# Performance work log

Hardware: AMD Instinct MI355X
Metric: run time of the kernel (lower is better)

The kernel has to match this reference:

```python
import jax, jax.numpy as jnp
import numpy as np

EPS_PROX = 5.0   # proximal epsilon from __init__
BN_EPS = 1e-5    # torch BatchNorm1d default eps
STRIDE = 3


def setup_inputs() -> dict:
    key = jax.random.key(0)
    ks = jax.random.split(key, 9)
    B, T, D = 64, 768, 128     # batch, timesteps, input_size
    E, H, O, K = 64, 128, 10, 3  # embedding_dim, hidden, output, kernel
    Tc = (T - K) // STRIDE + 1   # 256 conv output steps
    s_ih = 1.0 / np.sqrt(H)
    return {
        "inputs": jax.random.normal(ks[0], (B, T, D), jnp.float32),
        "r": jax.random.normal(ks[1], (B, E, Tc), jnp.float32),
        "conv_w": jax.random.normal(ks[2], (E, D, K), jnp.float32) * (1.0 / np.sqrt(D * K)),
        "conv_b": jnp.zeros((E,), jnp.float32),
        "bn_gamma": jnp.ones((E,), jnp.float32),
        "bn_beta": jnp.zeros((E,), jnp.float32),
        "w_ih": jax.random.normal(ks[3], (4 * H, E), jnp.float32) * s_ih,
        "w_hh": jax.random.normal(ks[4], (4 * H, H), jnp.float32) * s_ih,
        "b_ih": jax.random.normal(ks[5], (4 * H,), jnp.float32) * s_ih,
        "b_hh": jax.random.normal(ks[6], (4 * H,), jnp.float32) * s_ih,
        "lin_w": jax.random.normal(ks[7], (O, H), jnp.float32) * s_ih,
        "lin_b": jnp.zeros((O,), jnp.float32),
        "batch_size": B,
    }


def _forward(inputs, conv_w, conv_b, bn_gamma, bn_beta,
             w_ih, w_hh, b_ih, b_hh, lin_w, lin_b):
    # F.normalize(inputs, dim=2): L2 normalize feature dim
    nrm = jnp.sqrt(jnp.sum(inputs * inputs, axis=2, keepdims=True))
    x = inputs / jnp.maximum(nrm, 1e-12)
    x = jnp.transpose(x, (0, 2, 1))  # [B, D, T]
    # Conv1d(D -> E, kernel=3, stride=3)
    emb = jax.lax.conv_general_dilated(
        x, conv_w, window_strides=(STRIDE,), padding='VALID',
        dimension_numbers=('NCH', 'OIH', 'NCH')) + conv_b[None, :, None]
    # BatchNorm1d in training mode: batch stats over (B, T')
    mean = jnp.mean(emb, axis=(0, 2), keepdims=True)
    var = jnp.var(emb, axis=(0, 2), keepdims=True)
    emb = (emb - mean) * jax.lax.rsqrt(var + BN_EPS)
    emb = emb * bn_gamma[None, :, None] + bn_beta[None, :, None]
    act = jax.nn.relu(emb)               # [B, E, T']
    xs = jnp.transpose(act, (2, 0, 1))   # [T', B, E] scan over time

    H = w_hh.shape[1]
    Wi, Wf, Wg, Wo = jnp.split(w_ih, 4, axis=0)  # torch gate order i,f,g,o
    I_H = jnp.eye(H, dtype=inputs.dtype)

    def step(carry, x_t):
        h, c = carry
        z = x_t @ w_ih.T + b_ih + h @ w_hh.T + b_hh  # [B, 4H]
        zi, zf, zg, zo = jnp.split(z, 4, axis=1)
        i = jax.nn.sigmoid(zi)
        f = jax.nn.sigmoid(zf)
        g = jnp.tanh(zg)
        o = jax.nn.sigmoid(zo)
        s = f * c + i * g                            # pre-prox cell state
        # Analytic Jacobian G = ds/dx_t : [B, H, E]
        G = ((i * (1 - i) * g)[:, :, None] * Wi[None]
             + (f * (1 - f) * c)[:, :, None] * Wf[None]
             + (i * (1 - g * g))[:, :, None] * Wg[None])
        # Proximal update: c = (I + eps * G G^T)^{-1} s
        A = I_H + EPS_PROX * jnp.einsum('bhe,bke->bhk', G, G)
        c_new = jnp.linalg.solve(A, s[:, :, None])[:, :, 0]
        h_new = o * jnp.tanh(c_new)
        return (h_new, c_new), None

    B = xs.shape[1]
    init = (jnp.zeros((B, H), inputs.dtype), jnp.zeros((B, H), inputs.dtype))
    (h_last, _), _ = jax.lax.scan(step, init, xs)
    return h_last @ lin_w.T + lin_b  # [B, output_size]


def reference(inputs, r, conv_w, conv_b, bn_gamma, bn_beta,
              w_ih, w_hh, b_ih, b_hh, lin_w, lin_b, batch_size):
    # mode='ProxLSTM'; r and batch_size are unused in this branch (r is only
    # added to the embedding in 'plain' mode).
    return _forward(inputs, conv_w, conv_b, bn_gamma, bn_beta,
                    w_ih, w_hh, b_ih, b_hh, lin_w, lin_b)
```

## Files before the change

kernel.cpp:

```cpp
#include <hip/hip_runtime.h>
#include <math.h>

#define EPSP 5.0f
#define BNEPS 1e-5f
constexpr int B_  = 64;
constexpr int T_  = 768;
constexpr int D_  = 128;
constexpr int E_  = 64;
constexpr int H_  = 128;
constexpr int FH_ = 512;
constexpr int TC_ = 256;
constexpr int O_  = 10;

constexpr size_t EMB_OFF   = 0;
constexpr size_t SUM_OFF   = EMB_OFF + (size_t)B_ * TC_ * E_;
constexpr size_t SCL_OFF   = SUM_OFF + 128;
constexpr size_t CWT_OFF   = SCL_OFF + 128;
constexpr size_t WHIF_OFF  = CWT_OFF + (size_t)E_ * D_ * 3;
constexpr size_t WLO8F_OFF = WHIF_OFF + 32768;
constexpr size_t WTHI_OFF  = WLO8F_OFF + 16384;
constexpr size_t WTLO8_OFF = WTHI_OFF + 12288;
constexpr size_t ZX_OFF    = WTLO8_OFF + 6144;
constexpr size_t WS_FLOATS = ZX_OFF + (size_t)B_ * TC_ * FH_;

typedef __bf16 bf16x8 __attribute__((ext_vector_type(8)));
typedef float  floatx4 __attribute__((ext_vector_type(4)));

__device__ inline float fast_rcp(float x) { return __builtin_amdgcn_rcpf(x); }
__device__ inline float frsq(float x) { return __builtin_amdgcn_rsqf(x); }
__device__ inline float fexp2(float x) { return __builtin_amdgcn_exp2f(x); }
__device__ inline float rl(float v, int lane) {
  return __int_as_float(__builtin_amdgcn_readlane(__float_as_int(v), lane));
}
#define LOG2E 1.4426950408889634f
__device__ inline float fsigmoid(float x) { return fast_rcp(1.f + fexp2(-LOG2E * x)); }
__device__ inline float ftanh(float x) { return 1.f - 2.f * fast_rcp(1.f + fexp2(2.f * LOG2E * x)); }

__device__ inline unsigned char enc8(float v) {
  unsigned b = __float_as_uint(v);
  unsigned s = b >> 31;
  int e = (int)((b >> 23) & 0xFF) - 127;
  if (e < -6) return 0;
  unsigned m3 = (b >> 20) & 7;
  return (unsigned char)((s << 7) | ((unsigned)(e + 7) << 3) | m3);
}
#define S18 3.814697265625e-06f

__global__ void prep_kernel(const float* __restrict__ conv_w,
                            const float* __restrict__ w_hh,
                            float* __restrict__ ws) {
  int gid = blockIdx.x * blockDim.x + threadIdx.x;
  int nthr = gridDim.x * blockDim.x;
  for (int i = gid; i < 128; i += nthr) ws[SUM_OFF + i] = 0.f;
  __bf16* whiF = (__bf16*)(ws + WHIF_OFF);
  unsigned char* wlo8F = (unsigned char*)(ws + WLO8F_OFF);
  for (int s = gid; s < 512 * 128; s += nthr) {
    int st = s >> 7, r2 = s & 127, f = r2 >> 3, j = r2 & 7;
    int wv = st >> 6, lane = st & 63, m = lane & 15, q = lane >> 4;
    int rti = f >> 2, kt = f & 3;
    int R = wv * 64 + rti * 16 + m;
    int k = kt * 32 + q * 8 + j;
    float w = w_hh[(size_t)R * 128 + k];
    __bf16 hi = (__bf16)w;
    whiF[s] = hi;
    wlo8F[s] = enc8((w - (float)hi) * 16384.f);
  }
  for (int s = gid; s < E_ * D_ * 3; s += nthr) {
    int e = s / 384; int r = s - e * 384; int d = r / 3; int k = r - d * 3;
    ws[CWT_OFF + ((size_t)k * D_ + d) * E_ + e] = conv_w[s];
  }
}

__global__ __launch_bounds__(256) void conv_bn_kernel(const float* __restrict__ inputs,
                                                      const float* __restrict__ conv_b,
                                                      float* __restrict__ ws) {
  __shared__ float xin[48 * 129];
  __shared__ float rnorm[48];
  __shared__ float cwc[3 * 16 * 64];
  __shared__ float bnr1[256], bnr2[256];
  int tid = threadIdx.x;
  int bb = blockIdx.x >> 4, tcg = blockIdx.x & 15;
  const float* inp = inputs + ((size_t)bb * T_ + (size_t)tcg * 48) * D_;
  for (int idx = tid; idx < 48 * 128; idx += 256) {
    int r = idx >> 7, d = idx & 127;
    xin[r * 129 + d] = inp[idx];
  }
  __syncthreads();
  if (tid < 48) {
    float ss = 0.f;
    for (int d = 0; d < 128; ++d) { float v = xin[tid * 129 + d]; ss += v * v; }
    rnorm[tid] = 1.0f / fmaxf(sqrtf(ss), 1e-12f);
  }
  __syncthreads();
  for (int idx = tid; idx < 48 * 128; idx += 256) {
    int r = idx >> 7, d = idx & 127;
    xin[r * 129 + d] *= rnorm[r];
  }
  int e = tid & 63, tg = tid >> 6;
  float cb = conv_b[e];
  float acc[4];
#pragma unroll
  for (int q = 0; q < 4; ++q) acc[q] = cb;
  for (int ch = 0; ch < 8; ++ch) {
    __syncthreads();
    for (int idx = tid; idx < 3072; idx += 256) {
      int k = idx >> 10; int i2 = idx & 1023; int dd = i2 >> 6; int e2 = i2 & 63;
      cwc[idx] = ws[CWT_OFF + ((size_t)k * D_ + ch * 16 + dd) * E_ + e2];
    }
    __syncthreads();
    for (int dd = 0; dd < 16; ++dd) {
      int dcol = ch * 16 + dd;
#pragma unroll
      for (int k = 0; k < 3; ++k) {
        float w = cwc[(k * 16 + dd) * 64 + e];
#pragma unroll
        for (int q = 0; q < 4; ++q) {
          int tcl = tg * 4 + q;
          acc[q] += w * xin[(3 * tcl + k) * 129 + dcol];
        }
      }
    }
  }
  float ps = 0.f, pss = 0.f;
#pragma unroll
  for (int q = 0; q < 4; ++q) {
    int tcl = tg * 4 + q;
    ws[EMB_OFF + ((size_t)bb * TC_ + tcg * 16 + tcl) * E_ + e] = acc[q];
    ps += acc[q]; pss += acc[q] * acc[q];
  }
  bnr1[tg * 64 + e] = ps;
  bnr2[tg * 64 + e] = pss;
  __syncthreads();
  if (tid < 64) {
    float s1 = bnr1[tid] + bnr1[64 + tid] + bnr1[128 + tid] + bnr1[192 + tid];
    float s2 = bnr2[tid] + bnr2[64 + tid] + bnr2[128 + tid] + bnr2[192 + tid];
    atomicAdd(&ws[SUM_OFF + tid], s1);
    atomicAdd(&ws[SUM_OFF + 64 + tid], s2);
  }
}

__global__ void bn_finalize_kernel(const float* __restrict__ gamma,
                                   const float* __restrict__ beta,
                                   float* __restrict__ ws) {
  int e = threadIdx.x;
  if (e < 64) {
    const float n = (float)(B_ * TC_);
    float mean = ws[SUM_OFF + e] / n;
    float var = ws[SUM_OFF + 64 + e] / n - mean * mean;
    float sc = gamma[e] * rsqrtf(var + BNEPS);
    ws[SCL_OFF + e] = sc;
    ws[SCL_OFF + 64 + e] = beta[e] - mean * sc;
  }
}

__global__ __launch_bounds__(256) void zx_kernel(const float* __restrict__ w_ih,
                                                 const float* __restrict__ b_ih,
                                                 const float* __restrict__ b_hh,
                                                 float* __restrict__ ws) {
  __shared__ __align__(16) float actT[16 * 64];
  int tid = threadIdx.x;
  int bb = blockIdx.x >> 4, tg2 = blockIdx.x & 15;
  for (int idx = tid; idx < 1024; idx += 256) {
    int tl = idx >> 6, e2 = idx & 63;
    float v = ws[EMB_OFF + ((size_t)bb * TC_ + tg2 * 16 + tl) * E_ + e2];
    actT[idx] = fmaxf(v * ws[SCL_OFF + e2] + ws[SCL_OFF + 64 + e2], 0.f);
  }
  __syncthreads();
  int j0 = tid, j1 = tid + 256;
  float acc0[16], acc1[16];
  float bias0 = b_ih[j0] + b_hh[j0];
  float bias1 = b_ih[j1] + b_hh[j1];
#pragma unroll
  for (int tl = 0; tl < 16; ++tl) { acc0[tl] = bias0; acc1[tl] = bias1; }
  for (int e4 = 0; e4 < 16; ++e4) {
    float4 w0 = *(const float4*)(w_ih + (size_t)j0 * 64 + e4 * 4);
    float4 w1 = *(const float4*)(w_ih + (size_t)j1 * 64 + e4 * 4);
#pragma unroll
    for (int tl = 0; tl < 16; ++tl) {
      float4 a4 = *(const float4*)(actT + tl * 64 + e4 * 4);
      acc0[tl] += w0.x * a4.x + w0.y * a4.y + w0.z * a4.z + w0.w * a4.w;
      acc1[tl] += w1.x * a4.x + w1.y * a4.y + w1.z * a4.z + w1.w * a4.w;
    }
  }
#pragma unroll
  for (int tl = 0; tl < 16; ++tl) {
    size_t base = ZX_OFF + ((size_t)bb * TC_ + tg2 * 16 + tl) * FH_;
    ws[base + j0] = acc0[tl];
    ws[base + j1] = acc1[tl];
  }
}

template <int NCT>
__device__ inline void gram_do(int rt, int ct0, int lane,
                               const __bf16* GtHi, const __bf16* GtLo,
                               float* M_s, float* y_s) {
  int m = lane & 15, q = lane >> 4;
  bf16x8 AH[4], AL[4];
#pragma unroll
  for (int kt = 0; kt < 4; ++kt) {
    AH[kt] = *(const bf16x8*)(GtHi + (rt * 16 + m) * 136 + kt * 32 + q * 8);
    AL[kt] = *(const bf16x8*)(GtLo + (rt * 16 + m) * 136 + kt * 32 + q * 8);
  }
  floatx4 C[NCT];
#pragma unroll
  for (int ci = 0; ci < NCT; ++ci) C[ci] = (floatx4){0.f, 0.f, 0.f, 0.f};
#pragma unroll
  for (int ci = 0; ci < NCT; ++ci) {
#pragma unroll
    for (int kt = 0; kt < 4; ++kt) {
      bf16x8 BH = *(const bf16x8*)(GtHi + ((ct0 + ci) * 16 + m) * 136 + kt * 32 + q * 8);
      bf16x8 BL = *(const bf16x8*)(GtLo + ((ct0 + ci) * 16 + m) * 136 + kt * 32 + q * 8);
      C[ci] = __builtin_amdgcn_mfma_f32_16x16x32_bf16(AH[kt], BH, C[ci], 0, 0, 0);
      C[ci] = __builtin_amdgcn_mfma_f32_16x16x32_bf16(AH[kt], BL, C[ci], 0, 0, 0);
      C[ci] = __builtin_amdgcn_mfma_f32_16x16x32_bf16(AL[kt], BH, C[ci], 0, 0, 0);
    }
  }
#pragma unroll
  for (int ci = 0; ci < NCT; ++ci) {
    int ct = ct0 + ci;
#pragma unroll
    for (int reg = 0; reg < 4; ++reg) {
      int grow = rt * 16 + q * 4 + reg;
      if (ct < 4) {
        int gcol = ct * 16 + m;
        M_s[grow * 65 + gcol] = EPSP * C[ci][reg] + ((grow == gcol) ? 1.f : 0.f);
      } else if (m == 0) {
        y_s[grow] = C[ci][reg];
      }
    }
  }
}

#define LD8(dst, base) { float4 _a = *(const float4*)(base); float4 _b = *(const float4*)((base) + 4); \
  dst[0]=_a.x; dst[1]=_a.y; dst[2]=_a.z; dst[3]=_a.w; dst[4]=_b.x; dst[5]=_b.y; dst[6]=_b.z; dst[7]=_b.w; }

union U4L { uint4 u; long l[2]; };

__global__ __launch_bounds__(512, 2)
void scan_kernel(const float* __restrict__ w_ih,
                 const float* __restrict__ lin_w,
                 const float* __restrict__ lin_b,
                 const float* __restrict__ ws,
                 float* __restrict__ out) {
  __shared__ __align__(16) __bf16 GtHi[80 * 136], GtLo[80 * 136];
  __shared__ __align__(16) __bf16 hbH[128], hbL[128];
  __shared__ __align__(8)  unsigned char hb8[128];
  __shared__ float M_s[64 * 65];
  __shared__ float Lp_s[16 * 64];
  __shared__ __align__(16) float z0_s[512], zx_s[512];
  __shared__ __align__(16) float s_s[128], o_s[128], c_s[128], h_s[128];
  __shared__ float y_s[64];
  __shared__ __align__(8) float x_s[64];
  __shared__ __align__(16) unsigned char W8L[512 * 128];

  const int tid = threadIdx.x;
  const int bb = blockIdx.x;
  const int lane = tid & 63;
  const int wv = tid >> 6;
  const int m = lane & 15, q = lane >> 4;
  const int hg = tid >> 5;
  const int ep = tid & 31;
  const int h0 = hg * 8, e0 = ep * 2;

  float Wr[3][2][8];
#pragma unroll
  for (int g = 0; g < 3; ++g)
#pragma unroll
    for (int e = 0; e < 2; ++e) {
      const float* bse = w_ih + ((size_t)(g * 128 + h0)) * 64 + e0 + e;
#pragma unroll
      for (int r = 0; r < 8; ++r) Wr[g][e][r] = bse[(size_t)r * 64];
    }

  bf16x8 WH[4][4];
  {
    const uint4* whip = (const uint4*)(ws + WHIF_OFF) + (size_t)tid * 16;
#pragma unroll
    for (int rti = 0; rti < 4; ++rti)
#pragma unroll
      for (int kt = 0; kt < 4; ++kt) {
        uint4 t4 = whip[rti * 4 + kt];
        WH[rti][kt] = __builtin_bit_cast(bf16x8, t4);
      }
  }
  {
    const uint4* src = (const uint4*)(ws + WLO8F_OFF) + (size_t)tid * 8;
    uint4* dst = (uint4*)W8L;
#pragma unroll
    for (int f = 0; f < 8; ++f) dst[f * 512 + tid] = src[f];
  }
  for (int i = tid; i < 15 * 136; i += 512) { GtHi[65 * 136 + i] = (__bf16)0.f; GtLo[65 * 136 + i] = (__bf16)0.f; }
  if (tid < 128) {
    c_s[tid] = 0.f; h_s[tid] = 0.f;
    hbH[tid] = (__bf16)0.f; hbL[tid] = (__bf16)0.f; hb8[tid] = 0;
  }
  const float* zxp = ws + ZX_OFF + (size_t)bb * TC_ * FH_;
  float dinv = 1.f;
  bf16x8 ZB;
#pragma unroll
  for (int j = 0; j < 8; ++j) ZB[j] = (__bf16)0.f;
  float zxcur = zxp[tid];
  __syncthreads();

  for (int t = 0; t < TC_; ++t) {
    {
      zx_s[tid] = zxcur;
      if (t + 1 < TC_) zxcur = zxp[(size_t)(t + 1) * FH_ + tid];
      long B8[4];
#pragma unroll
      for (int kt = 0; kt < 4; ++kt)
        B8[kt] = (m == 0) ? *(const long*)(hb8 + kt * 32 + q * 8) : 0L;
      floatx4 C[4];
#pragma unroll
      for (int h2 = 0; h2 < 2; ++h2) {
        U4L wa[4];
#pragma unroll
        for (int i = 0; i < 4; ++i) wa[i].u = ((const uint4*)W8L)[(h2 * 4 + i) * 512 + tid];
        floatx4 C8a = {0,0,0,0}, C8b = {0,0,0,0};
#pragma unroll
        for (int kt = 0; kt < 4; ++kt) {
          long A0 = wa[(0 * 4 + kt) >> 1].l[kt & 1];
          long A1 = wa[(1 * 4 + kt) >> 1].l[kt & 1];
          C8a = __builtin_amdgcn_mfma_f32_16x16x32_fp8_fp8(A0, B8[kt], C8a, 0, 0, 0);
          C8b = __builtin_amdgcn_mfma_f32_16x16x32_fp8_fp8(A1, B8[kt], C8b, 0, 0, 0);
        }
        C[h2 * 2 + 0] = C8a * S18;
        C[h2 * 2 + 1] = C8b * S18;
      }
#pragma unroll
      for (int p = 0; p < 2; ++p) {
        const __bf16* hb = p ? hbL : hbH;
#pragma unroll
        for (int kt = 0; kt < 4; ++kt) {
          bf16x8 Bf = (m == 0) ? *(const bf16x8*)(hb + kt * 32 + q * 8) : ZB;
#pragma unroll
          for (int rti = 0; rti < 4; ++rti)
            C[rti] = __builtin_amdgcn_mfma_f32_16x16x32_bf16(WH[rti][kt], Bf, C[rti], 0, 0, 0);
        }
      }
      if (m == 0) {
#pragma unroll
        for (int rti = 0; rti < 4; ++rti)
          *(floatx4*)(z0_s + wv * 64 + rti * 16 + q * 4) = C[rti];
      }
    }
    __syncthreads();
    float gva[2][8];
    {
      float zA[8], xA[8], zi[8], zf[8], zg[8], zo[8], cc[8];
      LD8(zA, z0_s + h0) LD8(xA, zx_s + h0)
#pragma unroll
      for (int r = 0; r < 8; ++r) zi[r] = zA[r] + xA[r];
      LD8(zA, z0_s + 128 + h0) LD8(xA, zx_s + 128 + h0)
#pragma unroll
      for (int r = 0; r < 8; ++r) zf[r] = zA[r] + xA[r];
      LD8(zA, z0_s + 256 + h0) LD8(xA, zx_s + 256 + h0)
#pragma unroll
      for (int r = 0; r < 8; ++r) zg[r] = zA[r] + xA[r];
      LD8(zA, z0_s + 384 + h0) LD8(xA, zx_s + 384 + h0)
#pragma unroll
      for (int r = 0; r < 8; ++r) zo[r] = zA[r] + xA[r];
      LD8(cc, c_s + h0)
      float a1[8], a2[8], a3[8], sv[8], ov[8];
#pragma unroll
      for (int r = 0; r < 8; ++r) {
        float ig = fsigmoid(zi[r]);
        float fg = fsigmoid(zf[r]);
        float gg = ftanh(zg[r]);
        sv[r] = fg * cc[r] + ig * gg;
        ov[r] = fsigmoid(zo[r]);
        a1[r] = ig * (1.f - ig) * gg;
        a2[r] = fg * (1.f - fg) * cc[r];
        a3[r] = ig * (1.f - gg * gg);
      }
      if (ep == 0) {
        *(float4*)(s_s + h0)     = (float4){sv[0], sv[1], sv[2], sv[3]};
        *(float4*)(s_s + h0 + 4) = (float4){sv[4], sv[5], sv[6], sv[7]};
        *(float4*)(o_s + h0)     = (float4){ov[0], ov[1], ov[2], ov[3]};
        *(float4*)(o_s + h0 + 4) = (float4){ov[4], ov[5], ov[6], ov[7]};
        bf16x8 sh, sl;
#pragma unroll
        for (int r = 0; r < 8; ++r) {
          __bf16 hi = (__bf16)sv[r];
          sh[r] = hi; sl[r] = (__bf16)(sv[r] - (float)hi);
        }
        *(bf16x8*)(GtHi + 64 * 136 + h0) = sh;
        *(bf16x8*)(GtLo + 64 * 136 + h0) = sl;
      }
#pragma unroll
      for (int e = 0; e < 2; ++e) {
        int col = e0 + e;
        bf16x8 gh, gl;
#pragma unroll
        for (int r = 0; r < 8; ++r) {
          float gv = a1[r] * Wr[0][e][r] + a2[r] * Wr[1][e][r] + a3[r] * Wr[2][e][r];
          gva[e][r] = gv;
          __bf16 hi = (__bf16)gv;
          gh[r] = hi; gl[r] = (__bf16)(gv - (float)hi);
        }
        *(bf16x8*)(GtHi + col * 136 + h0) = gh;
        *(bf16x8*)(GtLo + col * 136 + h0) = gl;
      }
    }
    __syncthreads();
    if (wv < 4) gram_do<3>(wv, 0, lane, GtHi, GtLo, M_s, y_s);
    else        gram_do<2>(wv - 4, 3, lane, GtHi, GtLo, M_s, y_s);
    __syncthreads();
#pragma unroll 1
    for (int pan = 0; pan < 4; ++pan) {
      int j0 = pan * 16;
      if (tid < 64) {
        float p[16];
#pragma unroll
        for (int jj = 0; jj < 16; ++jj) p[jj] = M_s[lane * 65 + j0 + jj];
#pragma unroll
        for (int jj = 0; jj < 16; ++jj) {
          float d  = rl(p[jj], j0 + jj);
          float rs = frsq(d);
          p[jj] *= rs;
          dinv = (lane == j0 + jj) ? rs : dinv;
#pragma unroll
          for (int kk = jj + 1; kk < 16; ++kk) {
            float l = rl(p[jj], j0 + kk);
            p[kk] -= p[jj] * l;
          }
        }
#pragma unroll
        for (int jj = 0; jj < 16; ++jj) {
          M_s[lane * 65 + j0 + jj] = p[jj];
          Lp_s[jj * 64 + lane] = p[jj];
        }
        if (pan == 3) {
          float r = y_s[lane];
#pragma unroll 16
          for (int i = 0; i < 64; ++i) {
            float Lri = M_s[lane * 65 + i];
            float vv  = rl(r, i) * rl(dinv, i);
            float upd = r - Lri * vv;
            r = (lane == i) ? vv : ((lane > i) ? upd : r);
          }
#pragma unroll 16
          for (int i = 63; i >= 0; --i) {
            float Lil = M_s[i * 65 + lane];
            float vv  = rl(r, i) * rl(dinv, i);
            float upd = r - Lil * vv;
            r = (lane == i) ? vv : ((lane < i) ? upd : r);
          }
          x_s[lane] = r;
        }
      }
      __syncthreads();
      if (pan < 3) {
        float Lrow[16];
#pragma unroll
        for (int jj = 0; jj < 16; ++jj) Lrow[jj] = Lp_s[jj * 64 + lane];
        for (int k = j0 + 16 + wv; k < 64; k += 8) {
          float acc = M_s[lane * 65 + k];
#pragma unroll
          for (int jj = 0; jj < 16; ++jj) acc -= Lrow[jj] * Lp_s[jj * 64 + k];
          M_s[lane * 65 + k] = acc;
        }
        __syncthreads();
      }
    }
    {
      float2 xl = *(const float2*)(x_s + e0);
      float u0[8];
#pragma unroll
      for (int r = 0; r < 8; ++r) u0[r] = gva[0][r] * xl.x + gva[1][r] * xl.y;
#pragma unroll
      for (int sft = 1; sft < 32; sft <<= 1)
#pragma unroll
        for (int r = 0; r < 8; ++r) u0[r] += __shfl_xor(u0[r], sft, 32);
      if (ep == 0) {
        float cn[8], hn[8];
        bf16x8 hh8, hl8;
        unsigned long long h8v = 0ULL;
#pragma unroll
        for (int r = 0; r < 8; ++r) {
          cn[r] = s_s[h0 + r] - EPSP * u0[r];
          hn[r] = o_s[h0 + r] * ftanh(cn[r]);
          __bf16 hi = (__bf16)hn[r];
          hh8[r] = hi; hl8[r] = (__bf16)(hn[r] - (float)hi);
          h8v |= ((unsigned long long)enc8(hn[r] * 16.f)) << (8 * r);
        }
        *(float4*)(c_s + h0)     = (float4){cn[0], cn[1], cn[2], cn[3]};
        *(float4*)(c_s + h0 + 4) = (float4){cn[4], cn[5], cn[6], cn[7]};
        *(float4*)(h_s + h0)     = (float4){hn[0], hn[1], hn[2], hn[3]};
        *(float4*)(h_s + h0 + 4) = (float4){hn[4], hn[5], hn[6], hn[7]};
        *(bf16x8*)(hbH + h0) = hh8;
        *(bf16x8*)(hbL + h0) = hl8;
        *(unsigned long long*)(hb8 + h0) = h8v;
      }
    }
    __syncthreads();
  }
  if (tid < O_) {
    float acc = lin_b[tid];
    for (int hh2 = 0; hh2 < 128; ++hh2) acc += h_s[hh2] * lin_w[tid * 128 + hh2];
    out[(size_t)bb * O_ + tid] = acc;
  }
}

extern "C" void kernel_launch(void* const* d_in, const int* in_sizes, int n_in,
                              void* d_out, int out_size, void* d_ws, size_t ws_size,
                              hipStream_t stream) {
  (void)in_sizes; (void)n_in; (void)out_size;
  const float* inputs  = (const float*)d_in[0];
  const float* conv_w  = (const float*)d_in[2];
  const float* conv_b  = (const float*)d_in[3];
  const float* gamma   = (const float*)d_in[4];
  const float* beta    = (const float*)d_in[5];
  const float* w_ih    = (const float*)d_in[6];
  const float* w_hh    = (const float*)d_in[7];
  const float* b_ih    = (const float*)d_in[8];
  const float* b_hh    = (const float*)d_in[9];
  const float* lin_w   = (const float*)d_in[10];
  const float* lin_b   = (const float*)d_in[11];
  float* out = (float*)d_out;
  float* ws  = (float*)d_ws;

  if (ws_size < WS_FLOATS * sizeof(float)) return;

  hipLaunchKernelGGL(prep_kernel, dim3(192), dim3(256), 0, stream, conv_w, w_hh, ws);
  hipLaunchKernelGGL(conv_bn_kernel, dim3(1024), dim3(256), 0, stream, inputs, conv_b, ws);
  hipLaunchKernelGGL(bn_finalize_kernel, dim3(1), dim3(64), 0, stream, gamma, beta, ws);
  hipLaunchKernelGGL(zx_kernel, dim3(1024), dim3(256), 0, stream, w_ih, b_ih, b_hh, ws);
  hipLaunchKernelGGL(scan_kernel, dim3(64), dim3(512), 0, stream, w_ih, lin_w, lin_b, ws, out);
}
```

Baseline: 5.450 ms.

## Double scan kernel block to 1024 threads and halve per-thread recurrent work

The sequential scan kernel now runs 16 waves per batch element instead of 8. Each wave handles 32 rows of the recurrent matmul, each thread computes one Jacobian column for 8 hidden units, and the Gram work is split across 16 waves. The w_hh packing is changed to match the new wave layout. This shortens the per-step critical path by spreading work across more waves, at the cost of more barrier participants, a full-wave shuffle reduction, and idle threads in the serial Cholesky phases.

```diff
diff --git a/kernel.cpp b/kernel.cpp
--- a/kernel.cpp
+++ b/kernel.cpp
@@ -54,11 +54,11 @@
   for (int i = gid; i < 128; i += nthr) ws[SUM_OFF + i] = 0.f;
   __bf16* whiF = (__bf16*)(ws + WHIF_OFF);
   unsigned char* wlo8F = (unsigned char*)(ws + WLO8F_OFF);
-  for (int s = gid; s < 512 * 128; s += nthr) {
-    int st = s >> 7, r2 = s & 127, f = r2 >> 3, j = r2 & 7;
+  for (int s = gid; s < 1024 * 64; s += nthr) {
+    int st = s >> 6, r2 = s & 63, f = r2 >> 3, j = r2 & 7;
     int wv = st >> 6, lane = st & 63, m = lane & 15, q = lane >> 4;
     int rti = f >> 2, kt = f & 3;
-    int R = wv * 64 + rti * 16 + m;
+    int R = wv * 32 + rti * 16 + m;
     int k = kt * 32 + q * 8 + j;
     float w = w_hh[(size_t)R * 128 + k];
     __bf16 hi = (__bf16)w;
@@ -236,7 +236,7 @@
 
 union U4L { uint4 u; long l[2]; };
 
-__global__ __launch_bounds__(512, 2)
+__global__ __launch_bounds__(1024)
 void scan_kernel(const float* __restrict__ w_ih,
                  const float* __restrict__ lin_w,
                  const float* __restrict__ lin_b,
@@ -251,32 +251,29 @@
   __shared__ __align__(16) float s_s[128], o_s[128], c_s[128], h_s[128];
   __shared__ float y_s[64];
   __shared__ __align__(8) float x_s[64];
-  __shared__ __align__(16) unsigned char W8L[512 * 128];
+  __shared__ __align__(16) unsigned char W8L[4 * 1024 * 16];
 
   const int tid = threadIdx.x;
   const int bb = blockIdx.x;
   const int lane = tid & 63;
   const int wv = tid >> 6;
   const int m = lane & 15, q = lane >> 4;
-  const int hg = tid >> 5;
-  const int ep = tid & 31;
-  const int h0 = hg * 8, e0 = ep * 2;
-
-  float Wr[3][2][8];
-#pragma unroll
-  for (int g = 0; g < 3; ++g)
-#pragma unroll
-    for (int e = 0; e < 2; ++e) {
-      const float* bse = w_ih + ((size_t)(g * 128 + h0)) * 64 + e0 + e;
-#pragma unroll
-      for (int r = 0; r < 8; ++r) Wr[g][e][r] = bse[(size_t)r * 64];
-    }
-
-  bf16x8 WH[4][4];
+  const int h0 = wv * 8;
+  const int col = lane;
+
+  float Wr[3][8];
+#pragma unroll
+  for (int g = 0; g < 3; ++g) {
+    const float* bse = w_ih + ((size_t)(g * 128 + h0)) * 64 + col;
+#pragma unroll
+    for (int r = 0; r < 8; ++r) Wr[g][r] = bse[(size_t)r * 64];
+  }
+
+  bf16x8 WH[2][4];
   {
-    const uint4* whip = (const uint4*)(ws + WHIF_OFF) + (size_t)tid * 16;
-#pragma unroll
-    for (int rti = 0; rti < 4; ++rti)
+    const uint4* whip = (const uint4*)(ws + WHIF_OFF) + (size_t)tid * 8;
+#pragma unroll
+    for (int rti = 0; rti < 2; ++rti)
 #pragma unroll
       for (int kt = 0; kt < 4; ++kt) {
         uint4 t4 = whip[rti * 4 + kt];
@@ -284,12 +281,12 @@
       }
   }
   {
-    const uint4* src = (const uint4*)(ws + WLO8F_OFF) + (size_t)tid * 8;
+    const uint4* src = (const uint4*)(ws + WLO8F_OFF) + (size_t)tid * 4;
     uint4* dst = (uint4*)W8L;
 #pragma unroll
-    for (int f = 0; f < 8; ++f) dst[f * 512 + tid] = src[f];
-  }
-  for (int i = tid; i < 15 * 136; i += 512) { GtHi[65 * 136 + i] = (__bf16)0.f; GtLo[65 * 136 + i] = (__bf16)0.f; }
+    for (int f = 0; f < 4; ++f) dst[f * 1024 + tid] = src[f];
+  }
+  for (int i = tid; i < 15 * 136; i += 1024) { GtHi[65 * 136 + i] = (__bf16)0.f; GtLo[65 * 136 + i] = (__bf16)0.f; }
   if (tid < 128) {
     c_s[tid] = 0.f; h_s[tid] = 0.f;
     hbH[tid] = (__bf16)0.f; hbL[tid] = (__bf16)0.f; hb8[tid] = 0;
@@ -299,33 +296,34 @@
   bf16x8 ZB;
 #pragma unroll
   for (int j = 0; j < 8; ++j) ZB[j] = (__bf16)0.f;
-  float zxcur = zxp[tid];
+  float zxcur = (tid < 512) ? zxp[tid] : 0.f;
   __syncthreads();
 
   for (int t = 0; t < TC_; ++t) {
     {
-      zx_s[tid] = zxcur;
-      if (t + 1 < TC_) zxcur = zxp[(size_t)(t + 1) * FH_ + tid];
+      if (tid < 512) {
+        zx_s[tid] = zxcur;
+        if (t + 1 < TC_) zxcur = zxp[(size_t)(t + 1) * FH_ + tid];
+      }
       long B8[4];
 #pragma unroll
       for (int kt = 0; kt < 4; ++kt)
         B8[kt] = (m == 0) ? *(const long*)(hb8 + kt * 32 + q * 8) : 0L;
-      floatx4 C[4];
-#pragma unroll
-      for (int h2 = 0; h2 < 2; ++h2) {
+      floatx4 C[2];
+      {
         U4L wa[4];
 #pragma unroll
-        for (int i = 0; i < 4; ++i) wa[i].u = ((const uint4*)W8L)[(h2 * 4 + i) * 512 + tid];
-        floatx4 C8a = {0,0,0,0}, C8b = {0,0,0,0};
-#pragma unroll
-        for (int kt = 0; kt < 4; ++kt) {
-          long A0 = wa[(0 * 4 + kt) >> 1].l[kt & 1];
-          long A1 = wa[(1 * 4 + kt) >> 1].l[kt & 1];
-          C8a = __builtin_amdgcn_mfma_f32_16x16x32_fp8_fp8(A0, B8[kt], C8a, 0, 0, 0);
-          C8b = __builtin_amdgcn_mfma_f32_16x16x32_fp8_fp8(A1, B8[kt], C8b, 0, 0, 0);
-        }
-        C[h2 * 2 + 0] = C8a * S18;
-        C[h2 * 2 + 1] = C8b * S18;
+        for (int i = 0; i < 4; ++i) wa[i].u = ((const uint4*)W8L)[i * 1024 + tid];
+#pragma unroll
+        for (int rti = 0; rti < 2; ++rti) {
+          floatx4 C8 = {0, 0, 0, 0};
+#pragma unroll
+          for (int kt = 0; kt < 4; ++kt) {
+            long A0 = wa[(rti * 4 + kt) >> 1].l[kt & 1];
+            C8 = __builtin_amdgcn_mfma_f32_16x16x32_fp8_fp8(A0, B8[kt], C8, 0, 0, 0);
+          }
+          C[rti] = C8 * S18;
+        }
       }
 #pragma unroll
       for (int p = 0; p < 2; ++p) {
@@ -334,18 +332,18 @@
         for (int kt = 0; kt < 4; ++kt) {
           bf16x8 Bf = (m == 0) ? *(const bf16x8*)(hb + kt * 32 + q * 8) : ZB;
 #pragma unroll
-          for (int rti = 0; rti < 4; ++rti)
+          for (int rti = 0; rti < 2; ++rti)
             C[rti] = __builtin_amdgcn_mfma_f32_16x16x32_bf16(WH[rti][kt], Bf, C[rti], 0, 0, 0);
         }
       }
       if (m == 0) {
 #pragma unroll
-        for (int rti = 0; rti < 4; ++rti)
-          *(floatx4*)(z0_s + wv * 64 + rti * 16 + q * 4) = C[rti];
+        for (int rti = 0; rti < 2; ++rti)
+          *(floatx4*)(z0_s + wv * 32 + rti * 16 + q * 4) = C[rti];
       }
     }
     __syncthreads();
-    float gva[2][8];
+    float gva[8];
     {
       float zA[8], xA[8], zi[8], zf[8], zg[8], zo[8], cc[8];
       LD8(zA, z0_s + h0) LD8(xA, zx_s + h0)
@@ -373,7 +371,7 @@
         a2[r] = fg * (1.f - fg) * cc[r];
         a3[r] = ig * (1.f - gg * gg);
       }
-      if (ep == 0) {
+      if (lane == 0) {
         *(float4*)(s_s + h0)     = (float4){sv[0], sv[1], sv[2], sv[3]};
         *(float4*)(s_s + h0 + 4) = (float4){sv[4], sv[5], sv[6], sv[7]};
         *(float4*)(o_s + h0)     = (float4){ov[0], ov[1], ov[2], ov[3]};
@@ -387,14 +385,12 @@
         *(bf16x8*)(GtHi + 64 * 136 + h0) = sh;
         *(bf16x8*)(GtLo + 64 * 136 + h0) = sl;
       }
-#pragma unroll
-      for (int e = 0; e < 2; ++e) {
-        int col = e0 + e;
+      {
         bf16x8 gh, gl;
 #pragma unroll
         for (int r = 0; r < 8; ++r) {
-          float gv = a1[r] * Wr[0][e][r] + a2[r] * Wr[1][e][r] + a3[r] * Wr[2][e][r];
-          gva[e][r] = gv;
+          float gv = a1[r] * Wr[0][r] + a2[r] * Wr[1][r] + a3[r] * Wr[2][r];
+          gva[r] = gv;
           __bf16 hi = (__bf16)gv;
           gh[r] = hi; gl[r] = (__bf16)(gv - (float)hi);
         }
@@ -403,8 +399,11 @@
       }
     }
     __syncthreads();
-    if (wv < 4) gram_do<3>(wv, 0, lane, GtHi, GtLo, M_s, y_s);
-    else        gram_do<2>(wv - 4, 3, lane, GtHi, GtLo, M_s, y_s);
+    {
+      int rt = wv & 3, cs = wv >> 2;
+      if (cs < 3) gram_do<1>(rt, cs, lane, GtHi, GtLo, M_s, y_s);
+      else        gram_do<2>(rt, 3, lane, GtHi, GtLo, M_s, y_s);
+    }
     __syncthreads();
 #pragma unroll 1
     for (int pan = 0; pan < 4; ++pan) {
@@ -454,7 +453,7 @@
         float Lrow[16];
 #pragma unroll
         for (int jj = 0; jj < 16; ++jj) Lrow[jj] = Lp_s[jj * 64 + lane];
-        for (int k = j0 + 16 + wv; k < 64; k += 8) {
+        for (int k = j0 + 16 + wv; k < 64; k += 16) {
           float acc = M_s[lane * 65 + k];
 #pragma unroll
           for (int jj = 0; jj < 16; ++jj) acc -= Lrow[jj] * Lp_s[jj * 64 + k];
@@ -464,15 +463,15 @@
       }
     }
     {
-      float2 xl = *(const float2*)(x_s + e0);
+      float xl = x_s[col];
       float u0[8];
 #pragma unroll
-      for (int r = 0; r < 8; ++r) u0[r] = gva[0][r] * xl.x + gva[1][r] * xl.y;
-#pragma unroll
-      for (int sft = 1; sft < 32; sft <<= 1)
-#pragma unroll
-        for (int r = 0; r < 8; ++r) u0[r] += __shfl_xor(u0[r], sft, 32);
-      if (ep == 0) {
+      for (int r = 0; r < 8; ++r) u0[r] = gva[r] * xl;
+#pragma unroll
+      for (int sft = 1; sft < 64; sft <<= 1)
+#pragma unroll
+        for (int r = 0; r < 8; ++r) u0[r] += __shfl_xor(u0[r], sft, 64);
+      if (lane == 0) {
         float cn[8], hn[8];
         bf16x8 hh8, hl8;
         unsigned long long h8v = 0ULL;
@@ -526,5 +525,5 @@
   hipLaunchKernelGGL(conv_bn_kernel, dim3(1024), dim3(256), 0, stream, inputs, conv_b, ws);
   hipLaunchKernelGGL(bn_finalize_kernel, dim3(1), dim3(64), 0, stream, gamma, beta, ws);
   hipLaunchKernelGGL(zx_kernel, dim3(1024), dim3(256), 0, stream, w_ih, b_ih, b_hh, ws);
-  hipLaunchKernelGGL(scan_kernel, dim3(64), dim3(512), 0, stream, w_ih, lin_w, lin_b, ws, out);
-}
+  hipLaunchKernelGGL(scan_kernel, dim3(64), dim3(1024), 0, stream, w_ih, lin_w, lin_b, ws, out);
+}
```

Result: slower. 6.536 ms (+19.9%).

## Add look-ahead to blocked Cholesky and fold diagonal scaling into the solves

Applied to the files above, without the earlier changes.

The blocked Cholesky now updates only the next 16-column panel right after each panel is factored. The rest of the trailing update is deferred so warps 1-7 do it while warp 0 factors the following panel, with the panel buffer double-buffered to keep both in flight. The stored factor columns are pre-scaled by the inverse diagonal. This turns the forward and backward substitutions into simple multiply-subtract loops with a single diagonal scaling between them, in LDL^T style, removing per-step selects and reciprocal multiplies on the serial solve path. The cost is more complex indexing, more shared memory and a changed rounding order.

```diff
diff --git a/kernel.cpp b/kernel.cpp
--- a/kernel.cpp
+++ b/kernel.cpp
@@ -246,7 +246,7 @@
   __shared__ __align__(16) __bf16 hbH[128], hbL[128];
   __shared__ __align__(8)  unsigned char hb8[128];
   __shared__ float M_s[64 * 65];
-  __shared__ float Lp_s[16 * 64];
+  __shared__ float Lp2_s[2 * 16 * 64];
   __shared__ __align__(16) float z0_s[512], zx_s[512];
   __shared__ __align__(16) float s_s[128], o_s[128], c_s[128], h_s[128];
   __shared__ float y_s[64];
@@ -409,6 +409,8 @@
 #pragma unroll 1
     for (int pan = 0; pan < 4; ++pan) {
       int j0 = pan * 16;
+      float* Lpw = Lp2_s + (pan & 1) * (16 * 64);
+      float* Lpr = Lp2_s + (((pan & 1) ^ 1)) * (16 * 64);
       if (tid < 64) {
         float p[16];
 #pragma unroll
@@ -419,45 +421,54 @@
           float rs = frsq(d);
           p[jj] *= rs;
           dinv = (lane == j0 + jj) ? rs : dinv;
+          M_s[lane * 65 + j0 + jj] = (lane > j0 + jj) ? p[jj] * rs : 0.f;
+          Lpw[jj * 64 + lane] = p[jj];
 #pragma unroll
           for (int kk = jj + 1; kk < 16; ++kk) {
             float l = rl(p[jj], j0 + kk);
             p[kk] -= p[jj] * l;
           }
         }
-#pragma unroll
-        for (int jj = 0; jj < 16; ++jj) {
-          M_s[lane * 65 + j0 + jj] = p[jj];
-          Lp_s[jj * 64 + lane] = p[jj];
-        }
         if (pan == 3) {
           float r = y_s[lane];
 #pragma unroll 16
           for (int i = 0; i < 64; ++i) {
-            float Lri = M_s[lane * 65 + i];
-            float vv  = rl(r, i) * rl(dinv, i);
-            float upd = r - Lri * vv;
-            r = (lane == i) ? vv : ((lane > i) ? upd : r);
+            float Ai = M_s[lane * 65 + i];
+            r -= Ai * rl(r, i);
           }
+          float tau = r * dinv * dinv;
 #pragma unroll 16
           for (int i = 63; i >= 0; --i) {
-            float Lil = M_s[i * 65 + lane];
-            float vv  = rl(r, i) * rl(dinv, i);
-            float upd = r - Lil * vv;
-            r = (lane == i) ? vv : ((lane < i) ? upd : r);
+            float Bi = M_s[i * 65 + lane];
+            tau -= Bi * rl(tau, i);
           }
-          x_s[lane] = r;
+          x_s[lane] = tau;
+        }
+      } else if (pan >= 1) {
+        int k0 = 16 * pan + 16;
+        if (k0 < 64) {
+          float Lrow[16];
+#pragma unroll
+          for (int jj = 0; jj < 16; ++jj) Lrow[jj] = Lpr[jj * 64 + lane];
+          for (int k = k0 + (wv - 1); k < 64; k += 7) {
+            float acc = M_s[lane * 65 + k];
+#pragma unroll
+            for (int jj = 0; jj < 16; ++jj) acc -= Lrow[jj] * Lpr[jj * 64 + k];
+            M_s[lane * 65 + k] = acc;
+          }
         }
       }
       __syncthreads();
       if (pan < 3) {
         float Lrow[16];
 #pragma unroll
-        for (int jj = 0; jj < 16; ++jj) Lrow[jj] = Lp_s[jj * 64 + lane];
-        for (int k = j0 + 16 + wv; k < 64; k += 8) {
+        for (int jj = 0; jj < 16; ++jj) Lrow[jj] = Lpw[jj * 64 + lane];
+#pragma unroll
+        for (int kk2 = 0; kk2 < 2; ++kk2) {
+          int k = j0 + 16 + wv * 2 + kk2;
           float acc = M_s[lane * 65 + k];
 #pragma unroll
-          for (int jj = 0; jj < 16; ++jj) acc -= Lrow[jj] * Lp_s[jj * 64 + k];
+          for (int jj = 0; jj < 16; ++jj) acc -= Lrow[jj] * Lpw[jj * 64 + k];
           M_s[lane * 65 + k] = acc;
         }
         __syncthreads();
```

New measurement: 4.632 ms. 15.0% less time.
